# Kernel optimization log

Measured on AMD Instinct MI355X. Metric: run time of the kernel, lower is better.

## Reference

```python
import jax, jax.numpy as jnp
import numpy as np

# Model constants (from init_kwargs)
N_ATOMS = 30000
N_PAIRS = 300000
NF_IN = 64
NF_OUT = 64
N_DIST = 20
MIND_SOFT = 0.85
MAXD_SOFT = 5.0
HARD_CUTOFF = 6.5


def setup_inputs() -> dict:
    key = jax.random.key(0)
    k = jax.random.split(key, 8)
    in_features = jax.random.normal(k[0], (N_ATOMS, NF_IN), dtype=jnp.float32)
    pair_first = jax.random.randint(k[1], (N_PAIRS,), 0, N_ATOMS)
    pair_second = jax.random.randint(k[2], (N_PAIRS,), 0, N_ATOMS)
    dist_pairs = jax.random.uniform(k[3], (N_PAIRS,), dtype=jnp.float32,
                                    minval=MIND_SOFT, maxval=HARD_CUTOFF)
    # InverseSensitivityModule init: mu uniformly spaced in inverse-distance space
    mu = jnp.linspace(1.0 / MAXD_SOFT, 1.0 / MIND_SOFT, N_DIST, dtype=jnp.float32)
    sigma = jnp.full((N_DIST,), (1.0 / MIND_SOFT - 1.0 / MAXD_SOFT) / N_DIST,
                     dtype=jnp.float32)
    # xavier-normal-ish init scales
    int_weights = jax.random.normal(k[4], (N_DIST, NF_OUT, NF_IN), dtype=jnp.float32) \
        * np.sqrt(2.0 / (NF_IN + NF_OUT)).astype(np.float32)
    w_self = jax.random.normal(k[5], (NF_OUT, NF_IN), dtype=jnp.float32) \
        * np.sqrt(2.0 / (NF_IN + NF_OUT)).astype(np.float32)
    b_self = jax.random.normal(k[6], (NF_OUT,), dtype=jnp.float32) * 0.01
    return {"in_features": in_features, "pair_first": pair_first,
            "pair_second": pair_second, "dist_pairs": dist_pairs,
            "mu": mu, "sigma": sigma, "int_weights": int_weights,
            "w_self": w_self, "b_self": b_self}


def _sensitivity(dist, mu, sigma):
    # Inverse-distance Gaussian sensitivities with smooth cosine hard cutoff.
    inv_d = 1.0 / dist  # [P]
    gauss = jnp.exp(-0.5 * ((inv_d[:, None] - mu[None, :]) / sigma[None, :]) ** 2)  # [P, n_dist]
    cut = jnp.cos(0.5 * jnp.pi * dist / HARD_CUTOFF) ** 2
    cut = jnp.where(dist < HARD_CUTOFF, cut, 0.0)
    return gauss * cut[:, None]


def reference(in_features, pair_first, pair_second, dist_pairs,
              mu, sigma, int_weights, w_self, b_self):
    n_atoms = in_features.shape[0]
    sense = _sensitivity(dist_pairs, mu, sigma)              # [P, n_dist]
    # envsum: env[a, nu, f] = sum_{p: pair_first[p]==a} sense[p, nu] * in_features[pair_second[p], f]
    neigh = in_features[pair_second]                          # [P, nf_in] gather
    contrib = sense[:, :, None] * neigh[:, None, :]           # [P, n_dist, nf_in]
    env = jax.ops.segment_sum(
        contrib.reshape(contrib.shape[0], N_DIST * NF_IN),
        pair_first, num_segments=n_atoms)                     # [A, n_dist*nf_in]
    # interaction matmul: weights permuted (n_dist, nf_in, nf_out) then flattened
    weights_rs = jnp.transpose(int_weights, (0, 2, 1)).reshape(N_DIST * NF_IN, NF_OUT)
    features_out = env @ weights_rs                           # [A, nf_out]
    features_out += in_features @ w_self.T + b_self           # self interaction
    return features_out
```

## Files before the change

kernel.cpp:

```cpp
#include <hip/hip_runtime.h>
#include <math.h>

#define N_ATOMS    30000
#define N_PAIRS    300000
#define CAP        48
#define NF         64
#define ND         20
#define K_ENV      1280
#define K_TOT      1344
#define NKSTEP     42
#define HARD_CUT   6.5f
#define BA         16
#define ESTRIDE    1352
#define D_LO       0.85f
#define D_SCALE    (5.65f / 65535.0f)
#define D_SCALE_I  (65535.0f / 5.65f)

typedef short  s16x8  __attribute__((ext_vector_type(8)));
typedef __bf16 bf16x8 __attribute__((ext_vector_type(8)));
typedef float  f32x4  __attribute__((ext_vector_type(4)));
typedef float  f32x16 __attribute__((ext_vector_type(16)));

__device__ __forceinline__ unsigned short f2bf(float x) {
    union { float f; unsigned u; } v; v.f = x;
    unsigned r = v.u + 0x7fffu + ((v.u >> 16) & 1u);
    return (unsigned short)(r >> 16);
}
__device__ __forceinline__ unsigned pkbf(float a, float b) {
    return (unsigned)f2bf(a) | ((unsigned)f2bf(b) << 16);
}

__global__ void k_prep(const float* __restrict__ iw, const float* __restrict__ wself,
                       const float* __restrict__ mu, const float* __restrict__ sigma,
                       unsigned short* __restrict__ WtB, int* __restrict__ cnts,
                       float2* __restrict__ msr) {
    if (blockIdx.x < 42) {
        int idx = blockIdx.x * 256 + threadIdx.x;
        if (idx >= NKSTEP * 4 * 64) return;
        int l  = idx & 63;
        int q  = (idx >> 6) & 3;
        int ks = idx >> 8;
        int n  = q * 16 + (l & 15);
        int kb = ks * 32 + (l >> 4) * 8;
        union { unsigned short us[8]; uint4 v; } u;
        #pragma unroll
        for (int j = 0; j < 8; j++) {
            int k = kb + j;
            float val;
            if (k < K_ENV) {
                int t  = k / 640;
                int rm = k - t * 640;
                int g  = rm >> 7;
                int c  = (rm & 127) >> 2;
                int r  = k & 3;
                int nu = 4 * g + r;
                int f  = 32 * t + c;
                val = iw[(nu * NF + n) * NF + f];
            } else {
                val = wself[n * NF + (k - K_ENV)];
            }
            u.us[j] = f2bf(val);
        }
        *(uint4*)&WtB[idx * 8] = u.v;
    } else if (blockIdx.x < 160) {
        int i = (blockIdx.x - 42) * 256 + threadIdx.x;
        if (i < N_ATOMS) cnts[i] = 0;
    } else {
        int i = threadIdx.x;
        if (i < ND) { float2 m; m.x = mu[i]; m.y = 1.0f / sigma[i]; msr[i] = m; }
    }
}

__global__ void k_scatter(const int* __restrict__ first, const int* __restrict__ second,
                          const float* __restrict__ dist, int* __restrict__ cnts,
                          unsigned* __restrict__ pk) {
    int p = blockIdx.x * 256 + threadIdx.x;
    if (p >= N_PAIRS) return;
    int a = first[p];
    int pos = atomicAdd(&cnts[a], 1);
    if (pos < CAP) {
        float d = dist[p];
        unsigned du = (unsigned)((d - D_LO) * D_SCALE_I + 0.5f);
        du = min(du, 65535u);
        pk[(size_t)a * CAP + pos] = ((unsigned)second[p] << 16) | du;
    }
}

__global__ void __launch_bounds__(512, 6)
k_main(const float* __restrict__ x, const int* __restrict__ cnts,
       const unsigned* __restrict__ pk, const float2* __restrict__ msr,
       const unsigned short* __restrict__ WtB, const float* __restrict__ bself,
       float* __restrict__ out) {
    __shared__ unsigned short env[BA * ESTRIDE];
    const int t  = threadIdx.x;
    const int w  = t >> 6;
    const int l  = t & 63;
    const int h  = l >> 5;
    const int cl = l & 31;
    const int a0 = blockIdx.x * BA;

    float2 ms   = msr[min(cl, ND - 1)];
    const float isig  = ms.y;
    const float musig = ms.x * ms.y;
    const bool  nuok  = (cl < ND);

    for (int ci = 0; ci < 2; ci++) {
        const int i = 2 * w + ci;
        const int a = a0 + i;
        const int cnt = min(cnts[a], CAP);
        const int nst = max((cnt + 15) >> 4, 1);
        const unsigned* gb = &pk[(size_t)a * CAP];
        f32x16 acc0 = {0.f}, acc1 = {0.f};
        #pragma unroll 1
        for (int ks = 0; ks < nst; ks++) {
            const int k0 = ks * 16 + h * 8;
            uint4 p0 = *(const uint4*)(gb + k0);
            uint4 p1 = *(const uint4*)(gb + k0 + 4);
            unsigned pv[8] = {p0.x, p0.y, p0.z, p0.w, p1.x, p1.y, p1.z, p1.w};
            float bv0[8], bv1[8];
            #pragma unroll
            for (int j = 0; j < 8; j++) {
                unsigned idx = min(pv[j] >> 16, (unsigned)(N_ATOMS - 1));
                const float* xr = &x[idx * NF + cl];
                bv0[j] = xr[0];
                bv1[j] = xr[32];
            }
            union { unsigned u[4]; s16x8 s; } A, B0, B1;
            #pragma unroll
            for (int j = 0; j < 4; j++) {
                float e0, e1;
                {
                    float d   = D_LO + (float)(pv[2 * j] & 0xffffu) * D_SCALE;
                    float z   = __builtin_amdgcn_rcpf(d) * isig - musig;
                    float co  = __cosf(0.2416609733530613f * d);
                    float e   = __expf(-0.5f * z * z) * (co * co);
                    e0 = (nuok && (k0 + 2 * j) < cnt) ? e : 0.0f;
                }
                {
                    float d   = D_LO + (float)(pv[2 * j + 1] & 0xffffu) * D_SCALE;
                    float z   = __builtin_amdgcn_rcpf(d) * isig - musig;
                    float co  = __cosf(0.2416609733530613f * d);
                    float e   = __expf(-0.5f * z * z) * (co * co);
                    e1 = (nuok && (k0 + 2 * j + 1) < cnt) ? e : 0.0f;
                }
                A.u[j] = pkbf(e0, e1);
            }
            #pragma unroll
            for (int j = 0; j < 4; j++) {
                B0.u[j] = pkbf(bv0[2 * j], bv0[2 * j + 1]);
                B1.u[j] = pkbf(bv1[2 * j], bv1[2 * j + 1]);
            }
            acc0 = __builtin_amdgcn_mfma_f32_32x32x16_bf16(
                       __builtin_bit_cast(bf16x8, A.s),
                       __builtin_bit_cast(bf16x8, B0.s), acc0, 0, 0, 0);
            acc1 = __builtin_amdgcn_mfma_f32_32x32x16_bf16(
                       __builtin_bit_cast(bf16x8, A.s),
                       __builtin_bit_cast(bf16x8, B1.s), acc1, 0, 0, 0);
        }
        unsigned short* er = &env[i * ESTRIDE];
        #pragma unroll
        for (int q = 0; q < 3; q++) {
            int g = 2 * q + h;
            if (g < 5) {
                uint2 v0, v1;
                v0.x = pkbf(acc0[4 * q + 0], acc0[4 * q + 1]);
                v0.y = pkbf(acc0[4 * q + 2], acc0[4 * q + 3]);
                v1.x = pkbf(acc1[4 * q + 0], acc1[4 * q + 1]);
                v1.y = pkbf(acc1[4 * q + 2], acc1[4 * q + 3]);
                *(uint2*)&er[g * 128 + cl * 4]       = v0;
                *(uint2*)&er[640 + g * 128 + cl * 4] = v1;
            }
        }
        er[K_ENV + l] = f2bf(x[(size_t)a * NF + l]);
    }
    __syncthreads();

    if (w < 4) {
        const int m16  = l & 15;
        const int quad = l >> 4;
        f32x4 acc = {0.f, 0.f, 0.f, 0.f};
        for (int ks = 0; ks < NKSTEP; ks++) {
            s16x8 afrag = *(const s16x8*)&env[m16 * ESTRIDE + ks * 32 + quad * 8];
            s16x8 bfrag = *(const s16x8*)&WtB[((ks * 4 + w) * 64 + l) * 8];
            acc = __builtin_amdgcn_mfma_f32_16x16x32_bf16(
                      __builtin_bit_cast(bf16x8, afrag),
                      __builtin_bit_cast(bf16x8, bfrag), acc, 0, 0, 0);
        }
        const float bs = bself[w * 16 + m16];
        #pragma unroll
        for (int r = 0; r < 4; r++) {
            int row = quad * 4 + r;
            out[(size_t)(a0 + row) * NF + w * 16 + m16] = acc[r] + bs;
        }
    }
}

extern "C" void kernel_launch(void* const* d_in, const int* in_sizes, int n_in,
                              void* d_out, int out_size, void* d_ws, size_t ws_size,
                              hipStream_t stream) {
    const float* x      = (const float*)d_in[0];
    const int*   first  = (const int*)d_in[1];
    const int*   second = (const int*)d_in[2];
    const float* dist   = (const float*)d_in[3];
    const float* mu     = (const float*)d_in[4];
    const float* sigma  = (const float*)d_in[5];
    const float* iw     = (const float*)d_in[6];
    const float* wself  = (const float*)d_in[7];
    const float* bself  = (const float*)d_in[8];
    float* out = (float*)d_out;

    char* ws = (char*)d_ws;
    unsigned short* WtB  = (unsigned short*)(ws);
    int*            cnts = (int*)(ws + 172032);
    float2*         msr  = (float2*)(ws + 292032);
    unsigned*       pk   = (unsigned*)(ws + 292192);

    k_prep<<<dim3(161), dim3(256), 0, stream>>>(iw, wself, mu, sigma, WtB, cnts, msr);
    k_scatter<<<dim3((N_PAIRS + 255) / 256), dim3(256), 0, stream>>>(
        first, second, dist, cnts, pk);
    k_main<<<dim3(N_ATOMS / BA), dim3(512), 0, stream>>>(
        x, cnts, pk, msr, WtB, bself, out);
}
```

Measured before the change: 130.0 us.

## Use persistent blocks with atomic tile counter and float2 neighbor gathers

The main kernel now launches a fixed grid of persistent blocks that pull 16-atom tiles from a global atomic counter, replacing the one-block-per-tile launch. This is meant to balance the uneven per-atom pair counts and cut block launch overhead. Neighbor feature gathers now use a single float2 load per lane instead of two scalar loads. The weight layout is permuted to match the new interleaved feature order. The cost is an extra atomic and a block barrier per tile, and the loop relies on the counter being reset by the prep kernel on every call.

```diff
diff --git a/kernel.cpp b/kernel.cpp
--- a/kernel.cpp
+++ b/kernel.cpp
@@ -9,6 +9,8 @@
 #define K_ENV      1280
 #define K_TOT      1344
 #define NKSTEP     42
+#define NTILE      1875
+#define NBLK       768
 #define HARD_CUT   6.5f
 #define BA         16
 #define ESTRIDE    1352
@@ -33,7 +35,7 @@
 __global__ void k_prep(const float* __restrict__ iw, const float* __restrict__ wself,
                        const float* __restrict__ mu, const float* __restrict__ sigma,
                        unsigned short* __restrict__ WtB, int* __restrict__ cnts,
-                       float2* __restrict__ msr) {
+                       float2* __restrict__ msr, int* __restrict__ ctr) {
     if (blockIdx.x < 42) {
         int idx = blockIdx.x * 256 + threadIdx.x;
         if (idx >= NKSTEP * 4 * 64) return;
@@ -54,7 +56,7 @@
                 int c  = (rm & 127) >> 2;
                 int r  = k & 3;
                 int nu = 4 * g + r;
-                int f  = 32 * t + c;
+                int f  = 2 * c + t;
                 val = iw[(nu * NF + n) * NF + f];
             } else {
                 val = wself[n * NF + (k - K_ENV)];
@@ -68,6 +70,7 @@
     } else {
         int i = threadIdx.x;
         if (i < ND) { float2 m; m.x = mu[i]; m.y = 1.0f / sigma[i]; msr[i] = m; }
+        if (i == 0) *ctr = NBLK;
     }
 }
 
@@ -90,108 +93,117 @@
 k_main(const float* __restrict__ x, const int* __restrict__ cnts,
        const unsigned* __restrict__ pk, const float2* __restrict__ msr,
        const unsigned short* __restrict__ WtB, const float* __restrict__ bself,
-       float* __restrict__ out) {
+       float* __restrict__ out, int* __restrict__ ctr) {
     __shared__ unsigned short env[BA * ESTRIDE];
+    __shared__ int tile_s;
     const int t  = threadIdx.x;
     const int w  = t >> 6;
     const int l  = t & 63;
     const int h  = l >> 5;
     const int cl = l & 31;
-    const int a0 = blockIdx.x * BA;
+    const int m16  = l & 15;
+    const int quad = l >> 4;
 
     float2 ms   = msr[min(cl, ND - 1)];
     const float isig  = ms.y;
     const float musig = ms.x * ms.y;
     const bool  nuok  = (cl < ND);
-
-    for (int ci = 0; ci < 2; ci++) {
-        const int i = 2 * w + ci;
-        const int a = a0 + i;
-        const int cnt = min(cnts[a], CAP);
-        const int nst = max((cnt + 15) >> 4, 1);
-        const unsigned* gb = &pk[(size_t)a * CAP];
-        f32x16 acc0 = {0.f}, acc1 = {0.f};
-        #pragma unroll 1
-        for (int ks = 0; ks < nst; ks++) {
-            const int k0 = ks * 16 + h * 8;
-            uint4 p0 = *(const uint4*)(gb + k0);
-            uint4 p1 = *(const uint4*)(gb + k0 + 4);
-            unsigned pv[8] = {p0.x, p0.y, p0.z, p0.w, p1.x, p1.y, p1.z, p1.w};
-            float bv0[8], bv1[8];
+    const float bs = bself[(w & 3) * 16 + m16];
+
+    int tile = blockIdx.x;
+    for (;;) {
+        const int a0 = tile * BA;
+
+        for (int ci = 0; ci < 2; ci++) {
+            const int i = 2 * w + ci;
+            const int a = a0 + i;
+            const int cnt = min(cnts[a], CAP);
+            const int nst = max((cnt + 15) >> 4, 1);
+            const unsigned* gb = &pk[(size_t)a * CAP];
+            const float selfv = x[(size_t)a * NF + l];
+            f32x16 acc0 = {0.f}, acc1 = {0.f};
+            #pragma unroll 1
+            for (int ks = 0; ks < nst; ks++) {
+                const int k0 = ks * 16 + h * 8;
+                uint4 p0 = *(const uint4*)(gb + k0);
+                uint4 p1 = *(const uint4*)(gb + k0 + 4);
+                unsigned pv[8] = {p0.x, p0.y, p0.z, p0.w, p1.x, p1.y, p1.z, p1.w};
+                float2 bv[8];
+                #pragma unroll
+                for (int j = 0; j < 8; j++) {
+                    unsigned idx = min(pv[j] >> 16, (unsigned)(N_ATOMS - 1));
+                    bv[j] = *(const float2*)&x[idx * NF + 2 * cl];
+                }
+                union { unsigned u[4]; s16x8 s; } A, B0, B1;
+                #pragma unroll
+                for (int j = 0; j < 4; j++) {
+                    float e0, e1;
+                    {
+                        float d  = D_LO + (float)(pv[2 * j] & 0xffffu) * D_SCALE;
+                        float z  = __builtin_amdgcn_rcpf(d) * isig - musig;
+                        float co = __cosf(0.2416609733530613f * d);
+                        float e  = __expf(-0.5f * z * z) * (co * co);
+                        e0 = (nuok && (k0 + 2 * j) < cnt) ? e : 0.0f;
+                    }
+                    {
+                        float d  = D_LO + (float)(pv[2 * j + 1] & 0xffffu) * D_SCALE;
+                        float z  = __builtin_amdgcn_rcpf(d) * isig - musig;
+                        float co = __cosf(0.2416609733530613f * d);
+                        float e  = __expf(-0.5f * z * z) * (co * co);
+                        e1 = (nuok && (k0 + 2 * j + 1) < cnt) ? e : 0.0f;
+                    }
+                    A.u[j] = pkbf(e0, e1);
+                }
+                #pragma unroll
+                for (int j = 0; j < 4; j++) {
+                    B0.u[j] = pkbf(bv[2 * j].x, bv[2 * j + 1].x);
+                    B1.u[j] = pkbf(bv[2 * j].y, bv[2 * j + 1].y);
+                }
+                acc0 = __builtin_amdgcn_mfma_f32_32x32x16_bf16(
+                           __builtin_bit_cast(bf16x8, A.s),
+                           __builtin_bit_cast(bf16x8, B0.s), acc0, 0, 0, 0);
+                acc1 = __builtin_amdgcn_mfma_f32_32x32x16_bf16(
+                           __builtin_bit_cast(bf16x8, A.s),
+                           __builtin_bit_cast(bf16x8, B1.s), acc1, 0, 0, 0);
+            }
+            unsigned short* er = &env[i * ESTRIDE];
             #pragma unroll
-            for (int j = 0; j < 8; j++) {
-                unsigned idx = min(pv[j] >> 16, (unsigned)(N_ATOMS - 1));
-                const float* xr = &x[idx * NF + cl];
-                bv0[j] = xr[0];
-                bv1[j] = xr[32];
-            }
-            union { unsigned u[4]; s16x8 s; } A, B0, B1;
+            for (int q = 0; q < 3; q++) {
+                int g = 2 * q + h;
+                if (g < 5) {
+                    uint2 v0, v1;
+                    v0.x = pkbf(acc0[4 * q + 0], acc0[4 * q + 1]);
+                    v0.y = pkbf(acc0[4 * q + 2], acc0[4 * q + 3]);
+                    v1.x = pkbf(acc1[4 * q + 0], acc1[4 * q + 1]);
+                    v1.y = pkbf(acc1[4 * q + 2], acc1[4 * q + 3]);
+                    *(uint2*)&er[g * 128 + cl * 4]       = v0;
+                    *(uint2*)&er[640 + g * 128 + cl * 4] = v1;
+                }
+            }
+            er[K_ENV + l] = f2bf(selfv);
+        }
+        __syncthreads();
+
+        if (w < 4) {
+            f32x4 acc = {0.f, 0.f, 0.f, 0.f};
+            for (int ks = 0; ks < NKSTEP; ks++) {
+                s16x8 afrag = *(const s16x8*)&env[m16 * ESTRIDE + ks * 32 + quad * 8];
+                s16x8 bfrag = *(const s16x8*)&WtB[((ks * 4 + w) * 64 + l) * 8];
+                acc = __builtin_amdgcn_mfma_f32_16x16x32_bf16(
+                          __builtin_bit_cast(bf16x8, afrag),
+                          __builtin_bit_cast(bf16x8, bfrag), acc, 0, 0, 0);
+            }
             #pragma unroll
-            for (int j = 0; j < 4; j++) {
-                float e0, e1;
-                {
-                    float d   = D_LO + (float)(pv[2 * j] & 0xffffu) * D_SCALE;
-                    float z   = __builtin_amdgcn_rcpf(d) * isig - musig;
-                    float co  = __cosf(0.2416609733530613f * d);
-                    float e   = __expf(-0.5f * z * z) * (co * co);
-                    e0 = (nuok && (k0 + 2 * j) < cnt) ? e : 0.0f;
-                }
-                {
-                    float d   = D_LO + (float)(pv[2 * j + 1] & 0xffffu) * D_SCALE;
-                    float z   = __builtin_amdgcn_rcpf(d) * isig - musig;
-                    float co  = __cosf(0.2416609733530613f * d);
-                    float e   = __expf(-0.5f * z * z) * (co * co);
-                    e1 = (nuok && (k0 + 2 * j + 1) < cnt) ? e : 0.0f;
-                }
-                A.u[j] = pkbf(e0, e1);
-            }
-            #pragma unroll
-            for (int j = 0; j < 4; j++) {
-                B0.u[j] = pkbf(bv0[2 * j], bv0[2 * j + 1]);
-                B1.u[j] = pkbf(bv1[2 * j], bv1[2 * j + 1]);
-            }
-            acc0 = __builtin_amdgcn_mfma_f32_32x32x16_bf16(
-                       __builtin_bit_cast(bf16x8, A.s),
-                       __builtin_bit_cast(bf16x8, B0.s), acc0, 0, 0, 0);
-            acc1 = __builtin_amdgcn_mfma_f32_32x32x16_bf16(
-                       __builtin_bit_cast(bf16x8, A.s),
-                       __builtin_bit_cast(bf16x8, B1.s), acc1, 0, 0, 0);
+            for (int r = 0; r < 4; r++) {
+                int row = quad * 4 + r;
+                out[(size_t)(a0 + row) * NF + w * 16 + m16] = acc[r] + bs;
+            }
         }
-        unsigned short* er = &env[i * ESTRIDE];
-        #pragma unroll
-        for (int q = 0; q < 3; q++) {
-            int g = 2 * q + h;
-            if (g < 5) {
-                uint2 v0, v1;
-                v0.x = pkbf(acc0[4 * q + 0], acc0[4 * q + 1]);
-                v0.y = pkbf(acc0[4 * q + 2], acc0[4 * q + 3]);
-                v1.x = pkbf(acc1[4 * q + 0], acc1[4 * q + 1]);
-                v1.y = pkbf(acc1[4 * q + 2], acc1[4 * q + 3]);
-                *(uint2*)&er[g * 128 + cl * 4]       = v0;
-                *(uint2*)&er[640 + g * 128 + cl * 4] = v1;
-            }
-        }
-        er[K_ENV + l] = f2bf(x[(size_t)a * NF + l]);
-    }
-    __syncthreads();
-
-    if (w < 4) {
-        const int m16  = l & 15;
-        const int quad = l >> 4;
-        f32x4 acc = {0.f, 0.f, 0.f, 0.f};
-        for (int ks = 0; ks < NKSTEP; ks++) {
-            s16x8 afrag = *(const s16x8*)&env[m16 * ESTRIDE + ks * 32 + quad * 8];
-            s16x8 bfrag = *(const s16x8*)&WtB[((ks * 4 + w) * 64 + l) * 8];
-            acc = __builtin_amdgcn_mfma_f32_16x16x32_bf16(
-                      __builtin_bit_cast(bf16x8, afrag),
-                      __builtin_bit_cast(bf16x8, bfrag), acc, 0, 0, 0);
-        }
-        const float bs = bself[w * 16 + m16];
-        #pragma unroll
-        for (int r = 0; r < 4; r++) {
-            int row = quad * 4 + r;
-            out[(size_t)(a0 + row) * NF + w * 16 + m16] = acc[r] + bs;
-        }
+
+        if (t == 0) tile_s = atomicAdd(ctr, 1);
+        __syncthreads();
+        tile = tile_s;
+        if (tile >= NTILE) break;
     }
 }
 
@@ -213,11 +225,12 @@
     unsigned short* WtB  = (unsigned short*)(ws);
     int*            cnts = (int*)(ws + 172032);
     float2*         msr  = (float2*)(ws + 292032);
-    unsigned*       pk   = (unsigned*)(ws + 292192);
-
-    k_prep<<<dim3(161), dim3(256), 0, stream>>>(iw, wself, mu, sigma, WtB, cnts, msr);
+    int*            ctr  = (int*)(ws + 292192);
+    unsigned*       pk   = (unsigned*)(ws + 292256);
+
+    k_prep<<<dim3(161), dim3(256), 0, stream>>>(iw, wself, mu, sigma, WtB, cnts, msr, ctr);
     k_scatter<<<dim3((N_PAIRS + 255) / 256), dim3(256), 0, stream>>>(
         first, second, dist, cnts, pk);
-    k_main<<<dim3(N_ATOMS / BA), dim3(512), 0, stream>>>(
-        x, cnts, pk, msr, WtB, bself, out);
-}
+    k_main<<<dim3(NBLK), dim3(512), 0, stream>>>(
+        x, cnts, pk, msr, WtB, bself, out, ctr);
+}
```

After: 205.8 us. 1.58x slower.
